# Performance work log

Measured on AMD Instinct MI355X. Metric: run time of the kernel, lower is better.

Reference implementation:

```python
import jax, jax.numpy as jnp
import numpy as np

B, L, D, M, H = 32, 4096, 512, 64, 8
HD = D // H  # head dim = 64
NEG = -1e9


def setup_inputs() -> dict:
    key = jax.random.key(0)
    ks = jax.random.split(key, 12)
    s = 1.0 / np.sqrt(D)
    return {
        "query_features": jax.random.normal(ks[0], (B, L, D), jnp.float32),
        "mask": jax.random.randint(ks[1], (B, L), 0, 2, jnp.int32),
        "memory": jax.random.normal(ks[2], (M, D), jnp.float32),
        "Wq": jax.random.normal(ks[3], (D, D), jnp.float32) * s,
        "bq": jax.random.normal(ks[4], (D,), jnp.float32) * 0.01,
        "Wk": jax.random.normal(ks[5], (D, D), jnp.float32) * s,
        "bk": jax.random.normal(ks[6], (D,), jnp.float32) * 0.01,
        "Wv": jax.random.normal(ks[7], (D, D), jnp.float32) * s,
        "bv": jax.random.normal(ks[8], (D,), jnp.float32) * 0.01,
        "Wo": jax.random.normal(ks[9], (D, D), jnp.float32) * s,
        "bo": jax.random.normal(ks[10], (D,), jnp.float32) * 0.01,
    }


def reference(query_features, mask, memory, Wq, bq, Wk, bk, Wv, bv, Wo, bo):
    # read_memory: MHA(query=features, key=value=memory broadcast over batch)
    # with additive attn_mask of -1e9 on rows whose query position is invalid
    # (torch masks every key for an invalid query -> uniform attention there).
    q = (query_features @ Wq.T + bq).reshape(B, L, H, HD)
    k = (memory @ Wk.T + bk).reshape(M, H, HD)   # shared across batch
    v = (memory @ Wv.T + bv).reshape(M, H, HD)
    scores = jnp.einsum('blhd,mhd->bhlm', q, k) / np.sqrt(HD)  # [B,H,L,M]
    bias = jnp.where(mask[:, None, :, None] == 0, NEG, 0.0).astype(scores.dtype)
    attn = jax.nn.softmax(scores + bias, axis=-1)
    ctx = jnp.einsum('bhlm,mhd->blhd', attn, v).reshape(B, L, D)
    return ctx @ Wo.T + bo
```

## Files before the change

### kernel.cpp

```cpp
#include <hip/hip_runtime.h>
#include <hip/hip_bf16.h>

#define DD 512
#define HDIM 64
#define NROWS 131072

typedef __bf16 bf16x8 __attribute__((ext_vector_type(8)));
typedef float f32x4 __attribute__((ext_vector_type(4)));
typedef __bf16 bf16x2 __attribute__((ext_vector_type(2)));

static __device__ __forceinline__ unsigned bfbits(float f) {
    union { float f; unsigned u; } x; x.f = f;
    unsigned r = x.u + 0x7fffu + ((x.u >> 16) & 1u);
    return r >> 16;
}
static __device__ __forceinline__ __bf16 to_bf16(float f) {
    union { unsigned short s; __bf16 b; } y; y.s = (unsigned short)bfbits(f); return y.b;
}
static __device__ __forceinline__ unsigned pk2(float lo, float hi) {
    bf16x2 t; t[0] = (__bf16)lo; t[1] = (__bf16)hi;
    union { bf16x2 b; unsigned u; } z; z.b = t; return z.u;
}

static __device__ __forceinline__ int imgoff(int p, int g, int e) {
    return p * 64 + ((((g) ^ ((p) & 3) ^ (((p) >> 2) & 3)) & 3) << 4) + e * 2;
}

static __device__ __forceinline__ size_t fragoff(int c, int d) {
    return (size_t)((((c >> 6) * 64 + (d >> 5) * 4 + ((c >> 4) & 3)) << 10)
         + (((((d >> 3) & 3) << 4) + (c & 15)) << 4) + ((d & 7) << 1));
}

static __device__ __forceinline__ void gll16(const void* gsrc, void* ldst) {
    __builtin_amdgcn_global_load_lds(
        (const __attribute__((address_space(1))) unsigned int*)gsrc,
        (__attribute__((address_space(3))) unsigned int*)ldst, 16, 0, 0);
}

#define VMCNT(n) asm volatile("s_waitcnt vmcnt(" #n ")" ::: "memory")
#define LGKM0 asm volatile("s_waitcnt lgkmcnt(0)" ::: "memory")
#define MEMPIN asm volatile("" ::: "memory")

static __device__ __forceinline__ int xcd_swz(int bid, int nwg) {
    const int q = nwg >> 3, r = nwg & 7;
    const int xcd = bid & 7, idx = bid >> 3;
    return (xcd < r ? xcd * (q + 1) : r * (q + 1) + (xcd - r) * q) + idx;
}

__global__ void prep_kv(const float* __restrict__ memory,
                        const float* __restrict__ Wk, const float* __restrict__ bk,
                        const float* __restrict__ Wv, const float* __restrict__ bv,
                        float* __restrict__ kproj, float* __restrict__ vproj) {
    __shared__ float mrow[DD];
    const int m = blockIdx.x;
    const int t = threadIdx.x;
    for (int i = t; i < DD; i += 256) mrow[i] = memory[(size_t)m * DD + i];
    __syncthreads();
    for (int jj = 0; jj < 2; ++jj) {
        const int j = t + jj * 256;
        const float* wkr = Wk + (size_t)j * DD;
        const float* wvr = Wv + (size_t)j * DD;
        float sk = 0.f, sv = 0.f;
        for (int d = 0; d < DD; ++d) {
            const float md = mrow[d];
            sk += md * wkr[d];
            sv += md * wvr[d];
        }
        kproj[(size_t)m * DD + j] = sk + bk[j];
        vproj[(size_t)m * DD + j] = sv + bv[j];
    }
}

__global__ void prep_w(const float* __restrict__ Wq, const float* __restrict__ bq,
                       const float* __restrict__ Wo,
                       const float* __restrict__ kproj, const float* __restrict__ vproj,
                       char* __restrict__ W2img, float* __restrict__ b2,
                       char* __restrict__ W3fr) {
    const int i = blockIdx.x;
    const int t = threadIdx.x;
    __shared__ float kp[HDIM];
    __shared__ float worow[DD];
    const int m = i & 63, h = i >> 6;
    if (t < HDIM) kp[t] = kproj[(size_t)m * DD + h * HDIM + t];
    for (int d = t; d < DD; d += 256) worow[d] = Wo[(size_t)i * DD + d];
    __syncthreads();
    for (int dd2 = 0; dd2 < 2; ++dd2) {
        const int d = t + dd2 * 256;
        float s = 0.f;
        #pragma unroll 8
        for (int hd = 0; hd < HDIM; ++hd)
            s += Wq[(size_t)(h * HDIM + hd) * DD + d] * kp[hd];
        *(__bf16*)(W2img + (size_t)(d >> 5) * 32768 + imgoff(i, (d >> 3) & 3, d & 7)) = to_bf16(s);
    }
    if (t == 0) {
        float s = 0.f;
        for (int hd = 0; hd < HDIM; ++hd) s += bq[h * HDIM + hd] * kp[hd];
        b2[i] = s;
    }
    for (int cc = 0; cc < 2; ++cc) {
        const int c = t + cc * 256;
        const int mc = c & 63, hc = c >> 6;
        float s = 0.f;
        #pragma unroll 8
        for (int hd = 0; hd < HDIM; ++hd)
            s += vproj[(size_t)mc * DD + hc * HDIM + hd] * worow[hc * HDIM + hd];
        const int cp = (c & ~31) | (((c & 15) << 1) | ((c >> 4) & 1));
        *(__bf16*)(W3fr + fragoff(i, cp)) = to_bf16(s);
    }
}

__global__ __launch_bounds__(256, 2) void attn_fused(
    const float* __restrict__ x, const int* __restrict__ mask,
    const char* __restrict__ W2img, const float* __restrict__ b2,
    const char* __restrict__ W3fr, const float* __restrict__ bo,
    float* __restrict__ out) {
    __shared__ char ldsb[73728];

    const int tid = threadIdx.x;
    const int lane = tid & 63;
    const int wn = tid >> 6;
    const int lc = lane & 15, grp = lane >> 4;
    const int swz = xcd_swz(blockIdx.x, gridDim.x);
    const int gr0 = swz * 64;

    const int arow = tid >> 2, ag = tid & 3;
    const float* asrc = x + (size_t)(gr0 + arow) * DD + ag * 8;
    const int adst = imgoff(arow, ag, 0);
    const char* bsrc = W2img + wn * 8192 + lane * 16;

    f32x4 sreg[2][2];
    #define ALOAD(kt, set)                                                         \
        { sreg[set][0] = __builtin_nontemporal_load((const f32x4*)(asrc + (kt) * 32));     \
          sreg[set][1] = __builtin_nontemporal_load((const f32x4*)(asrc + (kt) * 32 + 4)); }
    #define AWRITE(buf, set)                                                       \
        { uint4 u;                                                                 \
          u.x = pk2(sreg[set][0][0], sreg[set][0][1]);                             \
          u.y = pk2(sreg[set][0][2], sreg[set][0][3]);                             \
          u.z = pk2(sreg[set][1][0], sreg[set][1][1]);                             \
          u.w = pk2(sreg[set][1][2], sreg[set][1][3]);                             \
          *(uint4*)(ldsb + (buf) * 4096 + adst) = u; }
    #define BGLL(kt, buf)                                                          \
        { _Pragma("unroll")                                                        \
          for (int g = 0; g < 8; ++g)                                              \
              gll16(bsrc + (size_t)(kt) * 32768 + g * 1024,                        \
                    ldsb + 8192 + (buf) * 32768 + wn * 8192 + g * 1024); }
    #define LDA1(buf, m)                                                           \
        (*(const bf16x8*)(ldsb + (buf) * 4096 + ((m) * 16 + lc) * 64               \
            + (((grp ^ (lc & 3) ^ (((m) * 4 + (lc >> 2)) & 3)) & 3) << 4)))
    #define LDB1(buf, n)                                                           \
        (*(const bf16x8*)(ldsb + 8192 + (buf) * 32768                              \
            + (wn * 128 + (n) * 16 + lc) * 64                                      \
            + (((grp ^ (lc & 3) ^ (((n) * 4 + (lc >> 2)) & 3)) & 3) << 4)))

    f32x4 acc[4][8];
    #pragma unroll
    for (int m = 0; m < 4; ++m)
        #pragma unroll
        for (int n = 0; n < 8; ++n) acc[m][n] = (f32x4){0.f, 0.f, 0.f, 0.f};

    BGLL(0, 0);
    MEMPIN;
    ALOAD(0, 0);
    MEMPIN;
    ALOAD(1, 1);
    VMCNT(2);
    AWRITE(0, 0);
    LGKM0;
    __builtin_amdgcn_s_barrier();
    __builtin_amdgcn_sched_barrier(0);

    #pragma unroll
    for (int s = 0; s < 16; ++s) {
        const int p = s & 1;
        if (s < 15) BGLL(s + 1, p ^ 1);
        MEMPIN;
        if (s < 14) ALOAD(s + 2, s & 1);
        bf16x8 af[4], bf[8];
        #pragma unroll
        for (int m = 0; m < 4; ++m) af[m] = LDA1(p, m);
        #pragma unroll
        for (int n = 0; n < 8; ++n) bf[n] = LDB1(p, n);
        __builtin_amdgcn_s_setprio(1);
        #pragma unroll
        for (int m = 0; m < 4; ++m)
            #pragma unroll
            for (int n = 0; n < 8; ++n)
                acc[m][n] = __builtin_amdgcn_mfma_f32_16x16x32_bf16(af[m], bf[n], acc[m][n], 0, 0, 0);
        __builtin_amdgcn_s_setprio(0);
        if (s < 14) {
            VMCNT(2);
            AWRITE(p ^ 1, (s + 1) & 1);
            LGKM0;
            __builtin_amdgcn_s_barrier();
            __builtin_amdgcn_sched_barrier(0);
        } else if (s < 15) {
            VMCNT(0);
            AWRITE(p ^ 1, 1);
            LGKM0;
            __builtin_amdgcn_s_barrier();
            __builtin_amdgcn_sched_barrier(0);
        }
    }
    __syncthreads();
    #undef ALOAD
    #undef AWRITE
    #undef BGLL
    #undef LDA1
    #undef LDB1

    const char* b3 = W3fr + wn * 131072 + lane * 16;
    #define LB3(kt, buf)                                                           \
        { _Pragma("unroll")                                                        \
          for (int n = 0; n < 8; ++n)                                              \
              bb3[buf][n] = *(const bf16x8*)(b3 + ((n) >> 2) * 65536               \
                  + (size_t)(kt) * 4096 + ((n) & 3) * 1024); }
    bf16x8 bb3[2][8];
    LB3(0, 0);

    float b2v[8];
    #pragma unroll
    for (int n = 0; n < 8; ++n) b2v[n] = b2[wn * 128 + n * 16 + lc];

    #pragma unroll
    for (int m = 0; m < 4; ++m) {
        const int4 mv = *(const int4*)(mask + gr0 + m * 16 + grp * 4);
        const int mk[4] = {mv.x, mv.y, mv.z, mv.w};
        #pragma unroll
        for (int hl = 0; hl < 2; ++hl) {
            #pragma unroll
            for (int j = 0; j < 4; ++j) {
                float s0 = (acc[m][hl * 4 + 0][j] + b2v[hl * 4 + 0]) * 0.125f;
                float s1 = (acc[m][hl * 4 + 1][j] + b2v[hl * 4 + 1]) * 0.125f;
                float s2 = (acc[m][hl * 4 + 2][j] + b2v[hl * 4 + 2]) * 0.125f;
                float s3 = (acc[m][hl * 4 + 3][j] + b2v[hl * 4 + 3]) * 0.125f;
                float mx = fmaxf(fmaxf(s0, s1), fmaxf(s2, s3));
                mx = fmaxf(mx, __shfl_xor(mx, 1));
                mx = fmaxf(mx, __shfl_xor(mx, 2));
                mx = fmaxf(mx, __shfl_xor(mx, 4));
                mx = fmaxf(mx, __shfl_xor(mx, 8));
                float p0 = __expf(s0 - mx);
                float p1 = __expf(s1 - mx);
                float p2 = __expf(s2 - mx);
                float p3 = __expf(s3 - mx);
                float sm = (p0 + p1) + (p2 + p3);
                sm += __shfl_xor(sm, 1);
                sm += __shfl_xor(sm, 2);
                sm += __shfl_xor(sm, 4);
                sm += __shfl_xor(sm, 8);
                float a0, a1, a2, a3;
                if (mk[j] == 0) {
                    a0 = a1 = a2 = a3 = 0.015625f;
                } else {
                    const float inv = 1.0f / sm;
                    a0 = p0 * inv; a1 = p1 * inv; a2 = p2 * inv; a3 = p3 * inv;
                }
                const int rl = m * 16 + grp * 4 + j;
                const int gp = ((lc >> 2) ^ (rl & 3) ^ ((rl >> 2) & 3)) & 3;
                const int base = 8192 + rl * 64 + (gp << 4) + (lc & 3) * 4;
                const int si0 = wn * 4 + hl * 2;
                *(unsigned*)(ldsb + base + si0 * 4096)       = pk2(a0, a1);
                *(unsigned*)(ldsb + base + (si0 + 1) * 4096) = pk2(a2, a3);
            }
        }
    }
    __syncthreads();

    #define LDA3(s, m)                                                             \
        (*(const bf16x8*)(ldsb + 8192 + (s) * 4096 + ((m) * 16 + lc) * 64          \
            + (((grp ^ (lc & 3) ^ (((m) * 4 + (lc >> 2)) & 3)) & 3) << 4)))

    #pragma unroll
    for (int m = 0; m < 4; ++m)
        #pragma unroll
        for (int n = 0; n < 8; ++n) acc[m][n] = (f32x4){0.f, 0.f, 0.f, 0.f};

    #pragma unroll
    for (int s = 0; s < 16; ++s) {
        const int p = s & 1;
        if (s < 15) LB3(s + 1, p ^ 1);
        bf16x8 af[4];
        #pragma unroll
        for (int m = 0; m < 4; ++m) af[m] = LDA3(s, m);
        __builtin_amdgcn_s_setprio(1);
        #pragma unroll
        for (int m = 0; m < 4; ++m)
            #pragma unroll
            for (int n = 0; n < 8; ++n)
                acc[m][n] = __builtin_amdgcn_mfma_f32_16x16x32_bf16(af[m], bb3[p][n], acc[m][n], 0, 0, 0);
        __builtin_amdgcn_s_setprio(0);
    }
    #undef LB3
    #undef LDA3

    float bov[8];
    #pragma unroll
    for (int n = 0; n < 8; ++n) bov[n] = bo[wn * 128 + n * 16 + lc];

    #pragma unroll
    for (int m = 0; m < 4; ++m) {
        #pragma unroll
        for (int j = 0; j < 4; ++j) {
            const int gr = gr0 + m * 16 + grp * 4 + j;
            float* orow = out + (size_t)gr * DD + wn * 128 + lc;
            #pragma unroll
            for (int n = 0; n < 8; ++n)
                __builtin_nontemporal_store(acc[m][n][j] + bov[n], orow + n * 16);
        }
    }
}

extern "C" void kernel_launch(void* const* d_in, const int* in_sizes, int n_in,
                              void* d_out, int out_size, void* d_ws, size_t ws_size,
                              hipStream_t stream) {
    const float* qf     = (const float*)d_in[0];
    const int*   mask   = (const int*)d_in[1];
    const float* memory = (const float*)d_in[2];
    const float* Wq     = (const float*)d_in[3];
    const float* bq     = (const float*)d_in[4];
    const float* Wk     = (const float*)d_in[5];
    const float* bk     = (const float*)d_in[6];
    const float* Wv     = (const float*)d_in[7];
    const float* bv     = (const float*)d_in[8];
    const float* Wo     = (const float*)d_in[9];
    const float* bo     = (const float*)d_in[10];

    char* ws = (char*)d_ws;
    float* kproj = (float*)ws;
    float* vproj = (float*)(ws + 131072);
    float* b2    = (float*)(ws + 262144);
    char*  W2img = ws + 264192;
    char*  W3fr  = ws + 788480;

    prep_kv<<<64, 256, 0, stream>>>(memory, Wk, bk, Wv, bv, kproj, vproj);
    prep_w<<<512, 256, 0, stream>>>(Wq, bq, Wo, kproj, vproj, W2img, b2, W3fr);
    attn_fused<<<NROWS / 64, 256, 0, stream>>>(qf, mask, W2img, b2, W3fr, bo, (float*)d_out);
}
```

Before: 288.5 us.

## Rewrite weight-prep kernels as LDS-tiled small GEMMs with vectorized bf16 stores

Rewrites prep_kv and prep_w as tiled matrix multiplies that stage memory, weight and projection tiles in padded LDS. Each thread now accumulates several outputs, where before each thread did strided global dot products. prep_w also packs eight bf16 results into one vector store to the W2/W3 image layouts. This targets the setup kernels' uncoalesced, low-reuse global reads, but it launches far fewer blocks (32 and 64), so the setup work may underuse the GPU. Its share of total time beside the large fused attention kernel is uncertain.

```diff
diff --git a/kernel.cpp b/kernel.cpp
--- a/kernel.cpp
+++ b/kernel.cpp
@@ -47,65 +47,144 @@
     return (xcd < r ? xcd * (q + 1) : r * (q + 1) + (xcd - r) * q) + idx;
 }
 
-__global__ void prep_kv(const float* __restrict__ memory,
-                        const float* __restrict__ Wk, const float* __restrict__ bk,
-                        const float* __restrict__ Wv, const float* __restrict__ bv,
-                        float* __restrict__ kproj, float* __restrict__ vproj) {
-    __shared__ float mrow[DD];
-    const int m = blockIdx.x;
+__global__ __launch_bounds__(256) void prep_kv(
+    const float* __restrict__ memory,
+    const float* __restrict__ Wk, const float* __restrict__ bk,
+    const float* __restrict__ Wv, const float* __restrict__ bv,
+    float* __restrict__ kproj, float* __restrict__ vproj) {
+    __shared__ float memLds[64 * 65];
+    __shared__ float wLds[32 * 65];
     const int t = threadIdx.x;
-    for (int i = t; i < DD; i += 256) mrow[i] = memory[(size_t)m * DD + i];
-    __syncthreads();
-    for (int jj = 0; jj < 2; ++jj) {
-        const int j = t + jj * 256;
-        const float* wkr = Wk + (size_t)j * DD;
-        const float* wvr = Wv + (size_t)j * DD;
-        float sk = 0.f, sv = 0.f;
-        for (int d = 0; d < DD; ++d) {
-            const float md = mrow[d];
-            sk += md * wkr[d];
-            sv += md * wvr[d];
-        }
-        kproj[(size_t)m * DD + j] = sk + bk[j];
-        vproj[(size_t)m * DD + j] = sv + bv[j];
-    }
-}
-
-__global__ void prep_w(const float* __restrict__ Wq, const float* __restrict__ bq,
-                       const float* __restrict__ Wo,
-                       const float* __restrict__ kproj, const float* __restrict__ vproj,
-                       char* __restrict__ W2img, float* __restrict__ b2,
-                       char* __restrict__ W3fr) {
-    const int i = blockIdx.x;
+    const int b = blockIdx.x;
+    const int mat = b >> 4;
+    const int j0 = (b & 15) * 32;
+    const float* W = mat ? Wv : Wk;
+    const float* bias = mat ? bv : bk;
+    float* proj = mat ? vproj : kproj;
+
+    const int jloc = t >> 3;
+    const int mbase = t & 7;
+    float acc[8] = {0.f, 0.f, 0.f, 0.f, 0.f, 0.f, 0.f, 0.f};
+
+    for (int dt = 0; dt < 8; ++dt) {
+        const int d0 = dt * 64;
+        __syncthreads();
+        #pragma unroll
+        for (int r = 0; r < 16; ++r) {
+            const int row = r * 4 + (t >> 6);
+            const int dd = t & 63;
+            memLds[row * 65 + dd] = memory[(size_t)row * DD + d0 + dd];
+        }
+        #pragma unroll
+        for (int r = 0; r < 8; ++r) {
+            const int row = r * 4 + (t >> 6);
+            const int dd = t & 63;
+            wLds[row * 65 + dd] = W[(size_t)(j0 + row) * DD + d0 + dd];
+        }
+        __syncthreads();
+        for (int d = 0; d < 64; ++d) {
+            const float wv = wLds[jloc * 65 + d];
+            #pragma unroll
+            for (int i = 0; i < 8; ++i)
+                acc[i] += memLds[(mbase + i * 8) * 65 + d] * wv;
+        }
+    }
+    const float bj = bias[j0 + jloc];
+    #pragma unroll
+    for (int i = 0; i < 8; ++i)
+        proj[(size_t)(mbase + i * 8) * DD + j0 + jloc] = acc[i] + bj;
+}
+
+__global__ __launch_bounds__(256) void prep_w(
+    const float* __restrict__ Wq, const float* __restrict__ bq,
+    const float* __restrict__ Wo,
+    const float* __restrict__ kproj, const float* __restrict__ vproj,
+    char* __restrict__ W2img, float* __restrict__ b2,
+    char* __restrict__ W3fr) {
+    __shared__ float aLds[64 * 65];
+    __shared__ float bLds[64 * 65];
     const int t = threadIdx.x;
-    __shared__ float kp[HDIM];
-    __shared__ float worow[DD];
-    const int m = i & 63, h = i >> 6;
-    if (t < HDIM) kp[t] = kproj[(size_t)m * DD + h * HDIM + t];
-    for (int d = t; d < DD; d += 256) worow[d] = Wo[(size_t)i * DD + d];
-    __syncthreads();
-    for (int dd2 = 0; dd2 < 2; ++dd2) {
-        const int d = t + dd2 * 256;
-        float s = 0.f;
-        #pragma unroll 8
-        for (int hd = 0; hd < HDIM; ++hd)
-            s += Wq[(size_t)(h * HDIM + hd) * DD + d] * kp[hd];
-        *(__bf16*)(W2img + (size_t)(d >> 5) * 32768 + imgoff(i, (d >> 3) & 3, d & 7)) = to_bf16(s);
-    }
-    if (t == 0) {
-        float s = 0.f;
-        for (int hd = 0; hd < HDIM; ++hd) s += bq[h * HDIM + hd] * kp[hd];
-        b2[i] = s;
-    }
-    for (int cc = 0; cc < 2; ++cc) {
-        const int c = t + cc * 256;
-        const int mc = c & 63, hc = c >> 6;
-        float s = 0.f;
-        #pragma unroll 8
-        for (int hd = 0; hd < HDIM; ++hd)
-            s += vproj[(size_t)mc * DD + hc * HDIM + hd] * worow[hc * HDIM + hd];
-        const int cp = (c & ~31) | (((c & 15) << 1) | ((c >> 4) & 1));
-        *(__bf16*)(W3fr + fragoff(i, cp)) = to_bf16(s);
+    const int b = blockIdx.x;
+
+    if (b < 32) {
+        const int h = b >> 2, dq = b & 3;
+        #pragma unroll
+        for (int r = 0; r < 16; ++r) {
+            const int row = r * 4 + (t >> 6), col = t & 63;
+            aLds[row * 65 + col] = kproj[(size_t)row * DD + h * 64 + col];
+        }
+        __syncthreads();
+        if (dq == 0 && t < 64) {
+            float s = 0.f;
+            for (int hd = 0; hd < 64; ++hd) s += bq[h * 64 + hd] * aLds[t * 65 + hd];
+            b2[h * 64 + t] = s;
+        }
+        for (int dt = 0; dt < 2; ++dt) {
+            const int d0 = dq * 128 + dt * 64;
+            __syncthreads();
+            #pragma unroll
+            for (int r = 0; r < 16; ++r) {
+                const int row = r * 4 + (t >> 6), col = t & 63;
+                bLds[row * 65 + col] = Wq[(size_t)(h * 64 + row) * DD + d0 + col];
+            }
+            __syncthreads();
+            #pragma unroll
+            for (int uu = 0; uu < 2; ++uu) {
+                const int u = t + 256 * uu;
+                const int m = u & 63, oct = u >> 6;
+                float acc[8] = {0.f, 0.f, 0.f, 0.f, 0.f, 0.f, 0.f, 0.f};
+                for (int hd = 0; hd < 64; ++hd) {
+                    const float kv = aLds[m * 65 + hd];
+                    #pragma unroll
+                    for (int e = 0; e < 8; ++e)
+                        acc[e] += kv * bLds[hd * 65 + oct * 8 + e];
+                }
+                const int d = d0 + oct * 8;
+                bf16x8 v;
+                #pragma unroll
+                for (int e = 0; e < 8; ++e) v[e] = to_bf16(acc[e]);
+                *(bf16x8*)(W2img + (size_t)(d >> 5) * 32768
+                           + imgoff(h * 64 + m, (d >> 3) & 3, 0)) = v;
+            }
+        }
+    } else {
+        const int hc = (b - 32) >> 2, jq = (b - 32) & 3;
+        #pragma unroll
+        for (int r = 0; r < 16; ++r) {
+            const int row = r * 4 + (t >> 6), col = t & 63;
+            aLds[row * 65 + col] = vproj[(size_t)row * DD + hc * 64 + col];
+        }
+        for (int jt = 0; jt < 2; ++jt) {
+            const int j0 = jq * 128 + jt * 64;
+            __syncthreads();
+            #pragma unroll
+            for (int r = 0; r < 16; ++r) {
+                const int row = r * 4 + (t >> 6), col = t & 63;
+                bLds[row * 65 + col] = Wo[(size_t)(j0 + row) * DD + hc * 64 + col];
+            }
+            __syncthreads();
+            #pragma unroll
+            for (int uu = 0; uu < 2; ++uu) {
+                const int u = t + 256 * uu;
+                const int jl = u & 63, w = u >> 6;
+                const int blk = w >> 2, oct = w & 3;
+                float acc[8] = {0.f, 0.f, 0.f, 0.f, 0.f, 0.f, 0.f, 0.f};
+                for (int hd = 0; hd < 64; ++hd) {
+                    const float wv = bLds[jl * 65 + hd];
+                    #pragma unroll
+                    for (int e = 0; e < 8; ++e) {
+                        const int s = oct * 8 + e;
+                        const int cl = (s >> 1) + ((s & 1) << 4);
+                        acc[e] += wv * aLds[(blk * 32 + cl) * 65 + hd];
+                    }
+                }
+                const int cp0 = hc * 64 + blk * 32 + oct * 8;
+                bf16x8 v;
+                #pragma unroll
+                for (int e = 0; e < 8; ++e) v[e] = to_bf16(acc[e]);
+                *(bf16x8*)(W3fr + fragoff(j0 + jl, cp0)) = v;
+            }
+        }
     }
 }
 
@@ -331,7 +410,7 @@
     char*  W2img = ws + 264192;
     char*  W3fr  = ws + 788480;
 
-    prep_kv<<<64, 256, 0, stream>>>(memory, Wk, bk, Wv, bv, kproj, vproj);
-    prep_w<<<512, 256, 0, stream>>>(Wq, bq, Wo, kproj, vproj, W2img, b2, W3fr);
+    prep_kv<<<32, 256, 0, stream>>>(memory, Wk, bk, Wv, bv, kproj, vproj);
+    prep_w<<<64, 256, 0, stream>>>(Wq, bq, Wo, kproj, vproj, W2img, b2, W3fr);
     attn_fused<<<NROWS / 64, 256, 0, stream>>>(qf, mask, W2img, b2, W3fr, bo, (float*)d_out);
 }
```

New measurement: 278.4 us. -3.5%, faster.
